# Optimization experiments

Measured on AMD Instinct MI355X. Metric: run time of the kernel, lower is better.

## Reference

```python
import jax, jax.numpy as jnp
import numpy as np

SCALE_BASE = 512.0
GN_EPS = 1e-5


def _xpos(x, downscale):
    # x: [..., L, D]; XPOS rotary embedding with exponential length scale (torchscale)
    L, D = x.shape[-2], x.shape[-1]
    half = D // 2
    base = (jnp.arange(0, D, 2, dtype=jnp.float32) + 0.4 * D) / (1.4 * D)  # [half]
    min_pos = -(L // 2)
    power = (jnp.arange(min_pos, min_pos + L, dtype=jnp.float32) / SCALE_BASE)[:, None]
    scale = base[None, :] ** power  # [L, half]
    inv_freq = 1.0 / (10000.0 ** (jnp.arange(half, dtype=jnp.float32) / half))
    ang = jnp.arange(L, dtype=jnp.float32)[:, None] * inv_freq[None, :]  # [L, half]
    sin, cos = jnp.sin(ang), jnp.cos(ang)
    if downscale:
        scale = 1.0 / scale
    sin_s = jnp.repeat(sin * scale, 2, axis=-1)  # duplicate_interleave -> [L, D]
    cos_s = jnp.repeat(cos * scale, 2, axis=-1)
    x1, x2 = x[..., ::2], x[..., 1::2]
    rot = jnp.stack((-x2, x1), axis=-1).reshape(x.shape)  # rotate_every_two
    return x * cos_s + rot * sin_s


def _decay_mask(L, H):
    gammas = 1.0 - jnp.exp(jnp.linspace(np.log(1.0 / 32.0), np.log(1.0 / 512.0), H)).astype(jnp.float32)
    idx = jnp.arange(L)
    dist = idx[:, None] - idx[None, :]  # [L, L]
    causal = dist >= 0
    d = jnp.maximum(dist, 0).astype(jnp.float32)
    # gamma^|n-s| below diagonal, 0 above (gamma^inf = 0 in the torch version)
    return jnp.where(causal[None], gammas[:, None, None] ** d[None], 0.0)  # [H, L, L]


def setup_inputs() -> dict:
    key = jax.random.key(0)
    ks = jax.random.split(key, 9)
    B, L, D, H = 2, 2048, 1024, 16
    hd = D // H
    return {
        "query": jax.random.normal(ks[0], (B, L, D), jnp.float32),
        "key": jax.random.normal(ks[1], (B, L, D), jnp.float32),
        "value": jax.random.normal(ks[2], (B, L, D), jnp.float32),
        "W_Q": jax.random.normal(ks[3], (H, D, hd), jnp.float32) / D,
        "W_K": jax.random.normal(ks[4], (H, D, hd), jnp.float32) / D,
        "W_V": jax.random.normal(ks[5], (H, D, hd), jnp.float32) / D,
        "g_w": jax.random.normal(ks[6], (D, D), jnp.float32) * (2.0 / (D + D)) ** 0.5,
        "g_b": jnp.zeros((D,), jnp.float32),
        "out_w": jax.random.normal(ks[7], (D, D), jnp.float32) * (2.0 / (D + D)) ** 0.5,
        "out_b": jnp.zeros((D,), jnp.float32),
    }


def reference(query, key, value, W_Q, W_K, W_V, g_w, g_b, out_w, out_b):
    B, L, D = query.shape
    H = W_Q.shape[0]
    q = jnp.einsum('bld,hde->bhle', query, W_Q)
    k = jnp.einsum('bld,hde->bhle', key, W_K)
    v = jnp.einsum('bld,hde->bhle', value, W_V)
    q = _xpos(q, downscale=False)
    k = _xpos(k, downscale=True)
    # retention_parallel: QK^T * decay mask (no softmax, no scale), then @ V
    sim = jnp.einsum('bhnd,bhsd->bhns', q, k) * _decay_mask(L, H)[None]
    ret = jnp.einsum('bhns,bhsd->bhnd', sim, v)  # [B, H, L, hd]
    # GroupNorm(num_groups=H, affine=False) on (b n, h d): normalize per (b, h, n) over hd
    mu = ret.mean(axis=-1, keepdims=True)
    var = ret.var(axis=-1, keepdims=True)
    ret = (ret - mu) / jnp.sqrt(var + GN_EPS)
    ret = ret.transpose(0, 2, 1, 3).reshape(B, L, D)  # b h n d -> b n (h d)
    gate = jax.nn.silu(query @ g_w.T + g_b)
    return (ret * gate) @ out_w.T + out_b
```

## Files before the change

### kernel.cpp

```cpp
#include <hip/hip_runtime.h>
#include <cstdint>

#define B_  2
#define L_  2048
#define D_  1024
#define H_  16
#define HD_ 64
#define M_  (B_*L_)

#define MD  4194304u
#define DD  1048576u

#define OFF_XQB  0u
#define OFF_XKB  (MD)
#define OFF_XVB  (2u*MD)
#define OFF_WQT  (3u*MD)
#define OFF_WKT  (3u*MD + DD)
#define OFF_WVT  (3u*MD + 2u*DD)
#define OFF_GWB  (3u*MD + 3u*DD)
#define OFF_OWB  (3u*MD + 4u*DD)
#define OFF_GATE (3u*MD + 5u*DD)
#define OFF_QB2  (OFF_GATE + MD)
#define OFF_KB2  (OFF_QB2 + MD)
#define OFF_VTG  (OFF_KB2 + MD)
#define OFF_ABUF (OFF_VTG + MD)
#define OFF_F32  (OFF_ABUF + MD)

typedef __attribute__((ext_vector_type(8))) short bf16x8;
typedef __attribute__((ext_vector_type(4))) float f32x4;

__device__ __forceinline__ unsigned short f2b(float x){
  union { float f; unsigned u; } a; a.f = x;
  unsigned r = a.u + 0x7FFFu + ((a.u >> 16) & 1u);
  return (unsigned short)(r >> 16);
}
__device__ __forceinline__ float b2f(unsigned short u){
  union { unsigned u; float f; } a; a.u = ((unsigned)u) << 16; return a.f;
}

__global__ __launch_bounds__(256) void cast_all_kernel(
    const float* __restrict__ q, const float* __restrict__ k,
    const float* __restrict__ v, const float* __restrict__ gw,
    const float* __restrict__ ow, unsigned short* __restrict__ ws)
{
  size_t i = ((size_t)blockIdx.x * 256 + threadIdx.x) * 4;
  const float* src; unsigned short* dst;
  if (i < MD)            { src = q  + i;              dst = ws + OFF_XQB + i; }
  else if (i < 2u*MD)    { src = k  + (i - MD);       dst = ws + OFF_XKB + (i - MD); }
  else if (i < 3u*MD)    { src = v  + (i - 2u*MD);    dst = ws + OFF_XVB + (i - 2u*MD); }
  else if (i < 3u*MD+DD) { src = gw + (i - 3u*MD);    dst = ws + OFF_GWB + (i - 3u*MD); }
  else                   { src = ow + (i - 3u*MD-DD); dst = ws + OFF_OWB + (i - 3u*MD - DD); }
  float4 vv = *(const float4*)src;
  ushort4 o; o.x = f2b(vv.x); o.y = f2b(vv.y); o.z = f2b(vv.z); o.w = f2b(vv.w);
  *(ushort4*)dst = o;
}

__global__ void transpose_w_kernel(const float* __restrict__ WQ,
                                   const float* __restrict__ WK,
                                   const float* __restrict__ WV,
                                   unsigned short* __restrict__ ws)
{
  __shared__ float t[32][33];
  const int z = blockIdx.z, w = z >> 4, h = z & 15;
  const float* in = (w == 0) ? WQ : (w == 1) ? WK : WV;
  unsigned short* out = ws + ((w == 0) ? OFF_WQT : (w == 1) ? OFF_WKT : OFF_WVT);
  const int d0 = blockIdx.x * 32, e0 = blockIdx.y * 32;
  const int x = threadIdx.x;
  for (int yy = threadIdx.y; yy < 32; yy += 8)
    t[yy][x] = in[((size_t)h * D_ + d0 + yy) * HD_ + e0 + x];
  __syncthreads();
  for (int yy = threadIdx.y; yy < 32; yy += 8)
    out[((size_t)h * HD_ + e0 + yy) * D_ + d0 + x] = f2b(t[x][yy]);
}

__global__ void xpos_tables_kernel(float* __restrict__ fb)
{
  const int l = blockIdx.x, i = threadIdx.x;
  const float base = (2.0f * (float)i + 0.4f * (float)HD_) / (1.4f * (float)HD_);
  const float p = (float)(l - L_ / 2) * (1.0f / 512.0f);
  const float sc = exp2f(p * log2f(base));
  const float invf = exp2f(-(float)i * (13.287712379549449f / 32.0f));
  float s, c; sincosf((float)l * invf, &s, &c);
  fb[          l * 32 + i] = c * sc;
  fb[ 65536 +  l * 32 + i] = s * sc;
  const float is = 1.0f / sc;
  fb[131072 +  l * 32 + i] = c * is;
  fb[196608 +  l * 32 + i] = s * is;
}

__device__ __forceinline__ void gemm_body(
    const unsigned short* __restrict__ A, const unsigned short* __restrict__ Bt,
    float* __restrict__ outF, unsigned short* __restrict__ outB,
    const float* __restrict__ ct, const float* __restrict__ st,
    const float* __restrict__ bias, int mode, int ldc, int M0, int N0,
    short* As, short* Bs)
{
  const int tid = threadIdx.x;
  const int wave = tid >> 6, lane = tid & 63;
  const int wm = wave & 1, wn = wave >> 1;
  const int mlane = lane & 15, kgrp = lane >> 4;
  const int arow0 = wave * 32 + (lane >> 2);
  const int akc   = lane & 3;
  const int brow  = wave * 16 + (lane >> 2);
  const char* Ab = (const char*)A;
  const char* Bb = (const char*)Bt;

  f32x4 acc[4][2] = {};

  for (int K0 = 0; K0 < 1024; K0 += 32) {
    __syncthreads();
#pragma unroll
    for (int t = 0; t < 2; ++t) {
      const char* g = Ab + ((size_t)(M0 + arow0 + t * 16) * 1024 + K0 + akc * 8) * 2;
      __builtin_amdgcn_global_load_lds(
          (const __attribute__((address_space(1))) void*)g,
          (__attribute__((address_space(3))) void*)((char*)As + (wave * 2 + t) * 1024 + lane * 16),
          16, 0, 0);
    }
    {
      const char* g = Bb + ((size_t)(N0 + brow) * 1024 + K0 + akc * 8) * 2;
      __builtin_amdgcn_global_load_lds(
          (const __attribute__((address_space(1))) void*)g,
          (__attribute__((address_space(3))) void*)((char*)Bs + wave * 1024 + lane * 16),
          16, 0, 0);
    }
    __syncthreads();
    bf16x8 af[4], bfr[2];
#pragma unroll
    for (int tm = 0; tm < 4; ++tm)
      af[tm] = *(const bf16x8*)&As[(wm * 64 + tm * 16 + mlane) * 32 + kgrp * 8];
#pragma unroll
    for (int tn = 0; tn < 2; ++tn)
      bfr[tn] = *(const bf16x8*)&Bs[(wn * 32 + tn * 16 + mlane) * 32 + kgrp * 8];
#pragma unroll
    for (int tm = 0; tm < 4; ++tm)
#pragma unroll
      for (int tn = 0; tn < 2; ++tn)
        acc[tm][tn] = __builtin_amdgcn_mfma_f32_16x16x32_bf16(af[tm], bfr[tn], acc[tm][tn], 0, 0, 0);
  }

#pragma unroll
  for (int tm = 0; tm < 4; ++tm)
#pragma unroll
    for (int tn = 0; tn < 2; ++tn) {
      f32x4 v = acc[tm][tn];
#pragma unroll
      for (int r = 0; r < 4; ++r) {
        const int grow = M0 + wm * 64 + tm * 16 + (lane >> 4) * 4 + r;
        const int gcol = N0 + wn * 32 + tn * 16 + mlane;
        float val = v[r];
        if (mode == 1 || mode == 2) {
          const float partner = __shfl_xor(val, 1);
          const int l = grow & (L_ - 1);
          const int i = (gcol >> 1) & 31;
          const float c = ct[l * 32 + i], s = st[l * 32 + i];
          val = (gcol & 1) ? (val * c + partner * s) : (val * c - partner * s);
          outB[(size_t)grow * ldc + gcol] = f2b(val);
        } else if (mode == 0) {
          outB[(size_t)grow * ldc + gcol] = f2b(val);
        } else if (mode == 3) {
          const float x = val + bias[gcol];
          outB[(size_t)grow * ldc + gcol] = f2b(x / (1.0f + expf(-x)));
        } else {
          outF[(size_t)grow * ldc + gcol] = val + bias[gcol];
        }
      }
    }
}

__global__ __launch_bounds__(256) void gemm4_kernel(
    unsigned short* __restrict__ ws, const float* __restrict__ g_b)
{
  __shared__ __align__(16) short As[128 * 32];
  __shared__ __align__(16) short Bs[64 * 32];
  const int z = blockIdx.y, bx = blockIdx.x;
  float* fb = (float*)(ws + OFF_F32);
  const unsigned short *A, *Bt; unsigned short* outB;
  const float *ct = nullptr, *st = nullptr, *bias = nullptr;
  int mode, ldc, M0, N0;
  if (z == 0) {
    A = ws + OFF_XQB; Bt = ws + OFF_WQT; outB = ws + OFF_QB2;
    ct = fb; st = fb + 65536; mode = 1; ldc = D_;
    M0 = (bx & 31) * 128; N0 = (bx >> 5) * 64;
  } else if (z == 1) {
    A = ws + OFF_XKB; Bt = ws + OFF_WKT; outB = ws + OFF_KB2;
    ct = fb + 131072; st = fb + 196608; mode = 2; ldc = D_;
    M0 = (bx & 31) * 128; N0 = (bx >> 5) * 64;
  } else if (z == 2) {
    A = ws + OFF_WVT; Bt = ws + OFF_XVB; outB = ws + OFF_VTG;
    mode = 0; ldc = M_;
    M0 = (bx & 7) * 128; N0 = (bx >> 3) * 64;
  } else {
    A = ws + OFF_XQB; Bt = ws + OFF_GWB; outB = ws + OFF_GATE;
    bias = g_b; mode = 3; ldc = D_;
    M0 = (bx & 31) * 128; N0 = (bx >> 5) * 64;
  }
  gemm_body(A, Bt, nullptr, outB, ct, st, bias, mode, ldc, M0, N0, As, Bs);
}

__global__ __launch_bounds__(256) void gemm_final_kernel(
    unsigned short* __restrict__ ws, const float* __restrict__ out_b,
    float* __restrict__ out)
{
  __shared__ __align__(16) short As[128 * 32];
  __shared__ __align__(16) short Bs[64 * 32];
  gemm_body(ws + OFF_ABUF, ws + OFF_OWB, out, nullptr, nullptr, nullptr,
            out_b, 4, D_, blockIdx.x * 128, blockIdx.y * 64, As, Bs);
}

#define QS_OFF 0
#define KS_OFF 16384
#define VT_OFF 24576
#define PS_OFF 32768

__global__ __launch_bounds__(256) void attn_mfma_kernel(
    const unsigned short* __restrict__ qg, const unsigned short* __restrict__ kg,
    const unsigned short* __restrict__ vtg, const unsigned short* __restrict__ gate,
    unsigned short* __restrict__ Abuf)
{
  __shared__ __align__(16) char smem[49152];
  const int tid = threadIdx.x, wave = tid >> 6, lane = tid & 63;
  const int mlane = lane & 15, kgrp = lane >> 4;
  const int id = blockIdx.x;
  const int bh = id & 31;
  const int u  = id >> 5;
  const int xq = (u < 8) ? u : (23 - u);
  const int l0 = xq * 128;
  const int b = bh >> 4, h = bh & 15;

  const float lo   = -3.4657359027997265f;
  const float step = -0.1848392481493187f;
  const float gamma = 1.0f - expf(lo + (float)h * step);
  const float lg2g  = log2f(gamma);
  const float g1    = exp2f(-lg2g);
  const float gmr[4] = {1.0f, g1, g1 * g1, g1 * g1 * g1};

  const int rl = lane >> 3, csel = lane & 7;

#pragma unroll
  for (int t = 0; t < 4; ++t) {
    const int row = 32 * wave + 8 * t + rl;
    const char* g = (const char*)(qg + (size_t)(b * L_ + l0 + row) * D_ + h * HD_ + ((csel ^ (row & 7)) << 3));
    __builtin_amdgcn_global_load_lds(
        (const __attribute__((address_space(1))) void*)g,
        (__attribute__((address_space(3))) void*)(smem + QS_OFF + (32 * wave + 8 * t) * 128 + lane * 16),
        16, 0, 0);
  }
  __syncthreads();

  bf16x8 qa[2][2];
#pragma unroll
  for (int tm = 0; tm < 2; ++tm)
#pragma unroll
    for (int kk = 0; kk < 2; ++kk) {
      const int row = 32 * wave + 16 * tm + mlane;
      qa[tm][kk] = *(const bf16x8*)(smem + QS_OFF + row * 128 + (((4 * kk + kgrp) ^ (row & 7)) << 4));
    }

  float rqm[2];
#pragma unroll
  for (int tm = 0; tm < 2; ++tm)
    rqm[tm] = exp2f((float)(l0 + 32 * wave + 16 * tm + mlane) * lg2g);

  f32x4 racc[2][4] = {};
  const int ntile = 2 * xq + 2;

  for (int it = 0; it < ntile; ++it) {
    const int s0 = it * 64;
    __syncthreads();
#pragma unroll
    for (int t = 0; t < 2; ++t) {
      const int row = 16 * wave + 8 * t + rl;
      const char* gk = (const char*)(kg + (size_t)(b * L_ + s0 + row) * D_ + h * HD_ + ((csel ^ (row & 7)) << 3));
      __builtin_amdgcn_global_load_lds(
          (const __attribute__((address_space(1))) void*)gk,
          (__attribute__((address_space(3))) void*)(smem + KS_OFF + (16 * wave + 8 * t) * 128 + lane * 16),
          16, 0, 0);
      const char* gv = (const char*)(vtg + (size_t)(h * HD_ + row) * M_ + b * L_ + s0 + ((csel ^ (row & 7)) << 3));
      __builtin_amdgcn_global_load_lds(
          (const __attribute__((address_space(1))) void*)gv,
          (__attribute__((address_space(3))) void*)(smem + VT_OFF + (16 * wave + 8 * t) * 128 + lane * 16),
          16, 0, 0);
    }
    __syncthreads();

    if (s0 <= l0 + 32 * wave + 31) {
      bf16x8 kb[4][2], vb[4][2];
#pragma unroll
      for (int tn = 0; tn < 4; ++tn)
#pragma unroll
        for (int kk = 0; kk < 2; ++kk) {
          const int row = 16 * tn + mlane;
          const int sw = ((4 * kk + kgrp) ^ (row & 7)) << 4;
          kb[tn][kk] = *(const bf16x8*)(smem + KS_OFF + row * 128 + sw);
          vb[tn][kk] = *(const bf16x8*)(smem + VT_OFF + row * 128 + sw);
        }
      float csb[4];
#pragma unroll
      for (int tn = 0; tn < 4; ++tn)
        csb[tn] = exp2f(-(float)(s0 + 16 * tn + 4 * kgrp) * lg2g);

#pragma unroll
      for (int tm = 0; tm < 2; ++tm) {
        const int rowmin = l0 + 32 * wave + 16 * tm;
        if (s0 > rowmin + 15) continue;
        f32x4 sf[4];
#pragma unroll
        for (int tn = 0; tn < 4; ++tn) {
          f32x4 z = {};
          z = __builtin_amdgcn_mfma_f32_16x16x32_bf16(kb[tn][0], qa[tm][0], z, 0, 0, 0);
          sf[tn] = __builtin_amdgcn_mfma_f32_16x16x32_bf16(kb[tn][1], qa[tm][1], z, 0, 0, 0);
        }
        const int nrow = rowmin + mlane;
        const bool needMask = (s0 + 63 >= rowmin);
        const int prow = 32 * wave + 16 * tm + mlane;
#pragma unroll
        for (int tn = 0; tn < 4; ++tn) {
          const float wbase = rqm[tm] * csb[tn];
          const int sbase = s0 + 16 * tn + 4 * kgrp;
          float vv[4];
#pragma unroll
          for (int r = 0; r < 4; ++r) {
            float w = wbase * gmr[r];
            if (needMask) w = (nrow - (sbase + r) >= 0) ? w : 0.0f;
            vv[r] = sf[tn][r] * w;
          }
          uint2 pk;
          pk.x = (unsigned)f2b(vv[0]) | ((unsigned)f2b(vv[1]) << 16);
          pk.y = (unsigned)f2b(vv[2]) | ((unsigned)f2b(vv[3]) << 16);
          *(uint2*)(smem + PS_OFF + prow * 128 +
                    (((2 * tn + (kgrp >> 1)) ^ (prow & 7)) << 4) + ((kgrp & 1) << 3)) = pk;
        }
        bf16x8 pa[2];
#pragma unroll
        for (int kk = 0; kk < 2; ++kk) {
          const int row = 32 * wave + 16 * tm + mlane;
          pa[kk] = *(const bf16x8*)(smem + PS_OFF + row * 128 + (((4 * kk + kgrp) ^ (row & 7)) << 4));
        }
#pragma unroll
        for (int tn = 0; tn < 4; ++tn) {
          racc[tm][tn] = __builtin_amdgcn_mfma_f32_16x16x32_bf16(pa[0], vb[tn][0], racc[tm][tn], 0, 0, 0);
          racc[tm][tn] = __builtin_amdgcn_mfma_f32_16x16x32_bf16(pa[1], vb[tn][1], racc[tm][tn], 0, 0, 0);
        }
      }
    }
  }

#pragma unroll
  for (int tm = 0; tm < 2; ++tm)
#pragma unroll
    for (int r = 0; r < 4; ++r) {
      float vv[4], sm = 0.0f, sq = 0.0f;
#pragma unroll
      for (int tn = 0; tn < 4; ++tn) {
        vv[tn] = racc[tm][tn][r];
        sm += vv[tn]; sq += vv[tn] * vv[tn];
      }
#pragma unroll
      for (int off = 1; off < 16; off <<= 1) {
        sm += __shfl_xor(sm, off);
        sq += __shfl_xor(sq, off);
      }
      const float mu = sm * (1.0f / 64.0f);
      float var = sq * (1.0f / 64.0f) - mu * mu;
      var = fmaxf(var, 0.0f);
      const float inv = rsqrtf(var + 1e-5f);
      const int row = l0 + 32 * wave + 16 * tm + kgrp * 4 + r;
      const size_t base = (size_t)(b * L_ + row) * D_ + h * HD_;
#pragma unroll
      for (int tn = 0; tn < 4; ++tn) {
        const int c = 16 * tn + mlane;
        const float g = b2f(gate[base + c]);
        Abuf[base + c] = f2b((vv[tn] - mu) * inv * g);
      }
    }
}

extern "C" void kernel_launch(void* const* d_in, const int* in_sizes, int n_in,
                              void* d_out, int out_size, void* d_ws, size_t ws_size,
                              hipStream_t stream)
{
  const float* query = (const float*)d_in[0];
  const float* key   = (const float*)d_in[1];
  const float* value = (const float*)d_in[2];
  const float* W_Q   = (const float*)d_in[3];
  const float* W_K   = (const float*)d_in[4];
  const float* W_V   = (const float*)d_in[5];
  const float* g_b   = (const float*)d_in[7];
  const float* out_b = (const float*)d_in[9];
  float* out = (float*)d_out;

  unsigned short* ws = (unsigned short*)d_ws;
  float* fb = (float*)(ws + OFF_F32);

  cast_all_kernel<<<14336, 256, 0, stream>>>(query, key, value,
                                             (const float*)d_in[6],
                                             (const float*)d_in[8], ws);
  transpose_w_kernel<<<dim3(32, 2, 48), dim3(32, 8), 0, stream>>>(W_Q, W_K, W_V, ws);
  xpos_tables_kernel<<<2048, 32, 0, stream>>>(fb);

  gemm4_kernel<<<dim3(512, 4), 256, 0, stream>>>(ws, g_b);

  attn_mfma_kernel<<<512, 256, 0, stream>>>(ws + OFF_QB2, ws + OFF_KB2,
                                            ws + OFF_VTG, ws + OFF_GATE,
                                            ws + OFF_ABUF);

  gemm_final_kernel<<<dim3(M_ / 128, D_ / 64), 256, 0, stream>>>(ws, out_b, out);
}
```

Before: 267.8 us.

## Fuse prep kernels, enlarge GEMM tiles to 128x128, persistent attention scheduler

Merges the cast, weight-transpose and xpos-table kernels into one launch to cut launch overhead. The GEMM tile grows from 128x64 to 128x128 with XOR-swizzled LDS to raise data reuse and avoid bank conflicts, at the cost of more accumulator registers and half as many blocks. Attention becomes a persistent kernel that takes 64-row query tiles from an atomic work counter, longest tiles first, to balance the causal triangle across CUs. The counter is reset inside the gemm4 kernel, which adds an ordering dependency between launches.

```diff
diff --git a/kernel.cpp b/kernel.cpp
--- a/kernel.cpp
+++ b/kernel.cpp
@@ -38,54 +38,55 @@
   union { unsigned u; float f; } a; a.u = ((unsigned)u) << 16; return a.f;
 }
 
-__global__ __launch_bounds__(256) void cast_all_kernel(
+__global__ __launch_bounds__(256) void prep_kernel(
     const float* __restrict__ q, const float* __restrict__ k,
     const float* __restrict__ v, const float* __restrict__ gw,
-    const float* __restrict__ ow, unsigned short* __restrict__ ws)
-{
-  size_t i = ((size_t)blockIdx.x * 256 + threadIdx.x) * 4;
-  const float* src; unsigned short* dst;
-  if (i < MD)            { src = q  + i;              dst = ws + OFF_XQB + i; }
-  else if (i < 2u*MD)    { src = k  + (i - MD);       dst = ws + OFF_XKB + (i - MD); }
-  else if (i < 3u*MD)    { src = v  + (i - 2u*MD);    dst = ws + OFF_XVB + (i - 2u*MD); }
-  else if (i < 3u*MD+DD) { src = gw + (i - 3u*MD);    dst = ws + OFF_GWB + (i - 3u*MD); }
-  else                   { src = ow + (i - 3u*MD-DD); dst = ws + OFF_OWB + (i - 3u*MD - DD); }
-  float4 vv = *(const float4*)src;
-  ushort4 o; o.x = f2b(vv.x); o.y = f2b(vv.y); o.z = f2b(vv.z); o.w = f2b(vv.w);
-  *(ushort4*)dst = o;
-}
-
-__global__ void transpose_w_kernel(const float* __restrict__ WQ,
-                                   const float* __restrict__ WK,
-                                   const float* __restrict__ WV,
-                                   unsigned short* __restrict__ ws)
+    const float* __restrict__ ow, const float* __restrict__ WQ,
+    const float* __restrict__ WK, const float* __restrict__ WV,
+    unsigned short* __restrict__ ws)
 {
   __shared__ float t[32][33];
-  const int z = blockIdx.z, w = z >> 4, h = z & 15;
-  const float* in = (w == 0) ? WQ : (w == 1) ? WK : WV;
-  unsigned short* out = ws + ((w == 0) ? OFF_WQT : (w == 1) ? OFF_WKT : OFF_WVT);
-  const int d0 = blockIdx.x * 32, e0 = blockIdx.y * 32;
-  const int x = threadIdx.x;
-  for (int yy = threadIdx.y; yy < 32; yy += 8)
-    t[yy][x] = in[((size_t)h * D_ + d0 + yy) * HD_ + e0 + x];
-  __syncthreads();
-  for (int yy = threadIdx.y; yy < 32; yy += 8)
-    out[((size_t)h * HD_ + e0 + yy) * D_ + d0 + x] = f2b(t[x][yy]);
-}
-
-__global__ void xpos_tables_kernel(float* __restrict__ fb)
-{
-  const int l = blockIdx.x, i = threadIdx.x;
-  const float base = (2.0f * (float)i + 0.4f * (float)HD_) / (1.4f * (float)HD_);
-  const float p = (float)(l - L_ / 2) * (1.0f / 512.0f);
-  const float sc = exp2f(p * log2f(base));
-  const float invf = exp2f(-(float)i * (13.287712379549449f / 32.0f));
-  float s, c; sincosf((float)l * invf, &s, &c);
-  fb[          l * 32 + i] = c * sc;
-  fb[ 65536 +  l * 32 + i] = s * sc;
-  const float is = 1.0f / sc;
-  fb[131072 +  l * 32 + i] = c * is;
-  fb[196608 +  l * 32 + i] = s * is;
+  const int bx = blockIdx.x, tid = threadIdx.x;
+  if (bx < 14336) {
+    size_t i = ((size_t)bx * 256 + tid) * 4;
+    const float* src; unsigned short* dst;
+    if (i < MD)            { src = q  + i;              dst = ws + OFF_XQB + i; }
+    else if (i < 2u*MD)    { src = k  + (i - MD);       dst = ws + OFF_XKB + (i - MD); }
+    else if (i < 3u*MD)    { src = v  + (i - 2u*MD);    dst = ws + OFF_XVB + (i - 2u*MD); }
+    else if (i < 3u*MD+DD) { src = gw + (i - 3u*MD);    dst = ws + OFF_GWB + (i - 3u*MD); }
+    else                   { src = ow + (i - 3u*MD-DD); dst = ws + OFF_OWB + (i - 3u*MD - DD); }
+    float4 vv = *(const float4*)src;
+    ushort4 o; o.x = f2b(vv.x); o.y = f2b(vv.y); o.z = f2b(vv.z); o.w = f2b(vv.w);
+    *(ushort4*)dst = o;
+  } else if (bx < 17408) {
+    const int tb = bx - 14336;
+    const int w = tb >> 10;
+    const int tb2 = tb & 1023;
+    const int h = tb2 >> 6, tt = tb2 & 63;
+    const int e0 = (tt & 1) * 32, d0 = (tt >> 1) * 32;
+    const float* in = (w == 0) ? WQ : (w == 1) ? WK : WV;
+    unsigned short* out = ws + ((w == 0) ? OFF_WQT : (w == 1) ? OFF_WKT : OFF_WVT);
+    const int x = tid & 31, y0 = tid >> 5;
+    for (int yy = y0; yy < 32; yy += 8)
+      t[yy][x] = in[((size_t)h * D_ + d0 + yy) * HD_ + e0 + x];
+    __syncthreads();
+    for (int yy = y0; yy < 32; yy += 8)
+      out[((size_t)h * HD_ + e0 + yy) * D_ + d0 + x] = f2b(t[x][yy]);
+  } else {
+    float* fb = (float*)(ws + OFF_F32);
+    const int idx = (bx - 17408) * 256 + tid;
+    const int l = idx >> 5, i = idx & 31;
+    const float base = (2.0f * (float)i + 0.4f * (float)HD_) / (1.4f * (float)HD_);
+    const float p = (float)(l - L_ / 2) * (1.0f / 512.0f);
+    const float sc = exp2f(p * log2f(base));
+    const float invf = exp2f(-(float)i * (13.287712379549449f / 32.0f));
+    float s, c; sincosf((float)l * invf, &s, &c);
+    fb[          l * 32 + i] = c * sc;
+    fb[ 65536 +  l * 32 + i] = s * sc;
+    const float is = 1.0f / sc;
+    fb[131072 +  l * 32 + i] = c * is;
+    fb[196608 +  l * 32 + i] = s * is;
+  }
 }
 
 __device__ __forceinline__ void gemm_body(
@@ -93,61 +94,64 @@
     float* __restrict__ outF, unsigned short* __restrict__ outB,
     const float* __restrict__ ct, const float* __restrict__ st,
     const float* __restrict__ bias, int mode, int ldc, int M0, int N0,
-    short* As, short* Bs)
+    char* As, char* Bs)
 {
   const int tid = threadIdx.x;
   const int wave = tid >> 6, lane = tid & 63;
   const int wm = wave & 1, wn = wave >> 1;
   const int mlane = lane & 15, kgrp = lane >> 4;
-  const int arow0 = wave * 32 + (lane >> 2);
-  const int akc   = lane & 3;
-  const int brow  = wave * 16 + (lane >> 2);
+  const int srow = lane >> 2;
+  const int scs  = lane & 3;
   const char* Ab = (const char*)A;
   const char* Bb = (const char*)Bt;
 
-  f32x4 acc[4][2] = {};
+  f32x4 acc[4][4] = {};
 
   for (int K0 = 0; K0 < 1024; K0 += 32) {
     __syncthreads();
 #pragma unroll
     for (int t = 0; t < 2; ++t) {
-      const char* g = Ab + ((size_t)(M0 + arow0 + t * 16) * 1024 + K0 + akc * 8) * 2;
+      const int row = wave * 32 + t * 16 + srow;
+      const int gc = scs ^ ((row >> 1) & 3);
+      const char* ga = Ab + ((size_t)(M0 + row) * 1024 + K0 + gc * 8) * 2;
       __builtin_amdgcn_global_load_lds(
-          (const __attribute__((address_space(1))) void*)g,
-          (__attribute__((address_space(3))) void*)((char*)As + (wave * 2 + t) * 1024 + lane * 16),
+          (const __attribute__((address_space(1))) void*)ga,
+          (__attribute__((address_space(3))) void*)(As + (wave * 32 + t * 16) * 64 + lane * 16),
           16, 0, 0);
-    }
-    {
-      const char* g = Bb + ((size_t)(N0 + brow) * 1024 + K0 + akc * 8) * 2;
+      const char* gb = Bb + ((size_t)(N0 + row) * 1024 + K0 + gc * 8) * 2;
       __builtin_amdgcn_global_load_lds(
-          (const __attribute__((address_space(1))) void*)g,
-          (__attribute__((address_space(3))) void*)((char*)Bs + wave * 1024 + lane * 16),
+          (const __attribute__((address_space(1))) void*)gb,
+          (__attribute__((address_space(3))) void*)(Bs + (wave * 32 + t * 16) * 64 + lane * 16),
           16, 0, 0);
     }
     __syncthreads();
-    bf16x8 af[4], bfr[2];
+    bf16x8 af[4], bfr[4];
+#pragma unroll
+    for (int tm = 0; tm < 4; ++tm) {
+      const int r = wm * 64 + tm * 16 + mlane;
+      af[tm] = *(const bf16x8*)(As + r * 64 + ((kgrp ^ ((r >> 1) & 3)) << 4));
+    }
+#pragma unroll
+    for (int tn = 0; tn < 4; ++tn) {
+      const int r = wn * 64 + tn * 16 + mlane;
+      bfr[tn] = *(const bf16x8*)(Bs + r * 64 + ((kgrp ^ ((r >> 1) & 3)) << 4));
+    }
 #pragma unroll
     for (int tm = 0; tm < 4; ++tm)
-      af[tm] = *(const bf16x8*)&As[(wm * 64 + tm * 16 + mlane) * 32 + kgrp * 8];
-#pragma unroll
-    for (int tn = 0; tn < 2; ++tn)
-      bfr[tn] = *(const bf16x8*)&Bs[(wn * 32 + tn * 16 + mlane) * 32 + kgrp * 8];
-#pragma unroll
-    for (int tm = 0; tm < 4; ++tm)
-#pragma unroll
-      for (int tn = 0; tn < 2; ++tn)
+#pragma unroll
+      for (int tn = 0; tn < 4; ++tn)
         acc[tm][tn] = __builtin_amdgcn_mfma_f32_16x16x32_bf16(af[tm], bfr[tn], acc[tm][tn], 0, 0, 0);
   }
 
 #pragma unroll
   for (int tm = 0; tm < 4; ++tm)
 #pragma unroll
-    for (int tn = 0; tn < 2; ++tn) {
+    for (int tn = 0; tn < 4; ++tn) {
       f32x4 v = acc[tm][tn];
 #pragma unroll
       for (int r = 0; r < 4; ++r) {
         const int grow = M0 + wm * 64 + tm * 16 + (lane >> 4) * 4 + r;
-        const int gcol = N0 + wn * 32 + tn * 16 + mlane;
+        const int gcol = N0 + wn * 64 + tn * 16 + mlane;
         float val = v[r];
         if (mode == 1 || mode == 2) {
           const float partner = __shfl_xor(val, 1);
@@ -171,29 +175,31 @@
 __global__ __launch_bounds__(256) void gemm4_kernel(
     unsigned short* __restrict__ ws, const float* __restrict__ g_b)
 {
-  __shared__ __align__(16) short As[128 * 32];
-  __shared__ __align__(16) short Bs[64 * 32];
+  __shared__ __align__(16) char As[128 * 64];
+  __shared__ __align__(16) char Bs[128 * 64];
   const int z = blockIdx.y, bx = blockIdx.x;
   float* fb = (float*)(ws + OFF_F32);
+  if (z == 0 && bx == 0 && threadIdx.x == 0)
+    ((unsigned*)(fb + 262144))[0] = 0;
   const unsigned short *A, *Bt; unsigned short* outB;
   const float *ct = nullptr, *st = nullptr, *bias = nullptr;
   int mode, ldc, M0, N0;
   if (z == 0) {
     A = ws + OFF_XQB; Bt = ws + OFF_WQT; outB = ws + OFF_QB2;
     ct = fb; st = fb + 65536; mode = 1; ldc = D_;
-    M0 = (bx & 31) * 128; N0 = (bx >> 5) * 64;
+    M0 = (bx & 31) * 128; N0 = (bx >> 5) * 128;
   } else if (z == 1) {
     A = ws + OFF_XKB; Bt = ws + OFF_WKT; outB = ws + OFF_KB2;
     ct = fb + 131072; st = fb + 196608; mode = 2; ldc = D_;
-    M0 = (bx & 31) * 128; N0 = (bx >> 5) * 64;
+    M0 = (bx & 31) * 128; N0 = (bx >> 5) * 128;
   } else if (z == 2) {
     A = ws + OFF_WVT; Bt = ws + OFF_XVB; outB = ws + OFF_VTG;
     mode = 0; ldc = M_;
-    M0 = (bx & 7) * 128; N0 = (bx >> 3) * 64;
+    M0 = (bx & 7) * 128; N0 = (bx >> 3) * 128;
   } else {
     A = ws + OFF_XQB; Bt = ws + OFF_GWB; outB = ws + OFF_GATE;
     bias = g_b; mode = 3; ldc = D_;
-    M0 = (bx & 31) * 128; N0 = (bx >> 5) * 64;
+    M0 = (bx & 31) * 128; N0 = (bx >> 5) * 128;
   }
   gemm_body(A, Bt, nullptr, outB, ct, st, bias, mode, ldc, M0, N0, As, Bs);
 }
@@ -202,89 +208,87 @@
     unsigned short* __restrict__ ws, const float* __restrict__ out_b,
     float* __restrict__ out)
 {
-  __shared__ __align__(16) short As[128 * 32];
-  __shared__ __align__(16) short Bs[64 * 32];
+  __shared__ __align__(16) char As[128 * 64];
+  __shared__ __align__(16) char Bs[128 * 64];
   gemm_body(ws + OFF_ABUF, ws + OFF_OWB, out, nullptr, nullptr, nullptr,
-            out_b, 4, D_, blockIdx.x * 128, blockIdx.y * 64, As, Bs);
-}
-
-#define QS_OFF 0
-#define KS_OFF 16384
-#define VT_OFF 24576
-#define PS_OFF 32768
+            out_b, 4, D_, blockIdx.x * 128, blockIdx.y * 128, As, Bs);
+}
+
+#define AQ_OFF 0
+#define AK_OFF 8192
+#define AV_OFF 16384
+#define AP_OFF 24576
 
 __global__ __launch_bounds__(256) void attn_mfma_kernel(
     const unsigned short* __restrict__ qg, const unsigned short* __restrict__ kg,
     const unsigned short* __restrict__ vtg, const unsigned short* __restrict__ gate,
-    unsigned short* __restrict__ Abuf)
-{
-  __shared__ __align__(16) char smem[49152];
+    unsigned short* __restrict__ Abuf, unsigned* __restrict__ ctr)
+{
+  __shared__ __align__(16) char smem[32768];
+  __shared__ unsigned s_item;
   const int tid = threadIdx.x, wave = tid >> 6, lane = tid & 63;
   const int mlane = lane & 15, kgrp = lane >> 4;
-  const int id = blockIdx.x;
-  const int bh = id & 31;
-  const int u  = id >> 5;
-  const int xq = (u < 8) ? u : (23 - u);
-  const int l0 = xq * 128;
-  const int b = bh >> 4, h = bh & 15;
+  const int rl = lane >> 3, csel = lane & 7;
 
   const float lo   = -3.4657359027997265f;
   const float step = -0.1848392481493187f;
-  const float gamma = 1.0f - expf(lo + (float)h * step);
-  const float lg2g  = log2f(gamma);
-  const float g1    = exp2f(-lg2g);
-  const float gmr[4] = {1.0f, g1, g1 * g1, g1 * g1 * g1};
-
-  const int rl = lane >> 3, csel = lane & 7;
-
-#pragma unroll
-  for (int t = 0; t < 4; ++t) {
-    const int row = 32 * wave + 8 * t + rl;
-    const char* g = (const char*)(qg + (size_t)(b * L_ + l0 + row) * D_ + h * HD_ + ((csel ^ (row & 7)) << 3));
-    __builtin_amdgcn_global_load_lds(
-        (const __attribute__((address_space(1))) void*)g,
-        (__attribute__((address_space(3))) void*)(smem + QS_OFF + (32 * wave + 8 * t) * 128 + lane * 16),
-        16, 0, 0);
-  }
-  __syncthreads();
-
-  bf16x8 qa[2][2];
-#pragma unroll
-  for (int tm = 0; tm < 2; ++tm)
-#pragma unroll
-    for (int kk = 0; kk < 2; ++kk) {
-      const int row = 32 * wave + 16 * tm + mlane;
-      qa[tm][kk] = *(const bf16x8*)(smem + QS_OFF + row * 128 + (((4 * kk + kgrp) ^ (row & 7)) << 4));
-    }
-
-  float rqm[2];
-#pragma unroll
-  for (int tm = 0; tm < 2; ++tm)
-    rqm[tm] = exp2f((float)(l0 + 32 * wave + 16 * tm + mlane) * lg2g);
-
-  f32x4 racc[2][4] = {};
-  const int ntile = 2 * xq + 2;
-
-  for (int it = 0; it < ntile; ++it) {
-    const int s0 = it * 64;
-    __syncthreads();
+
+  for (;;) {
+    __syncthreads();
+    if (tid == 0) s_item = atomicAdd(ctr, 1u);
+    __syncthreads();
+    const unsigned j = s_item;
+    if (j >= 1024u) break;
+    const int xq = 31 - (int)(j >> 5);
+    const int bh = (int)(j & 31u), b = bh >> 4, h = bh & 15;
+    const int l0 = xq * 64;
+
+    const float gamma = 1.0f - expf(lo + (float)h * step);
+    const float lg2g  = log2f(gamma);
+    const float g1    = exp2f(-lg2g);
+    const float gmr[4] = {1.0f, g1, g1 * g1, g1 * g1 * g1};
+
 #pragma unroll
     for (int t = 0; t < 2; ++t) {
       const int row = 16 * wave + 8 * t + rl;
-      const char* gk = (const char*)(kg + (size_t)(b * L_ + s0 + row) * D_ + h * HD_ + ((csel ^ (row & 7)) << 3));
+      const char* g = (const char*)(qg + (size_t)(b * L_ + l0 + row) * D_ + h * HD_ + ((csel ^ (row & 7)) << 3));
       __builtin_amdgcn_global_load_lds(
-          (const __attribute__((address_space(1))) void*)gk,
-          (__attribute__((address_space(3))) void*)(smem + KS_OFF + (16 * wave + 8 * t) * 128 + lane * 16),
+          (const __attribute__((address_space(1))) void*)g,
+          (__attribute__((address_space(3))) void*)(smem + AQ_OFF + (16 * wave + 8 * t) * 128 + lane * 16),
           16, 0, 0);
-      const char* gv = (const char*)(vtg + (size_t)(h * HD_ + row) * M_ + b * L_ + s0 + ((csel ^ (row & 7)) << 3));
-      __builtin_amdgcn_global_load_lds(
-          (const __attribute__((address_space(1))) void*)gv,
-          (__attribute__((address_space(3))) void*)(smem + VT_OFF + (16 * wave + 8 * t) * 128 + lane * 16),
-          16, 0, 0);
-    }
-    __syncthreads();
-
-    if (s0 <= l0 + 32 * wave + 31) {
+    }
+    __syncthreads();
+
+    bf16x8 qa[2];
+    {
+      const int row = 16 * wave + mlane;
+#pragma unroll
+      for (int kk = 0; kk < 2; ++kk)
+        qa[kk] = *(const bf16x8*)(smem + AQ_OFF + row * 128 + (((4 * kk + kgrp) ^ (row & 7)) << 4));
+    }
+    const float rqm = exp2f((float)(l0 + 16 * wave + mlane) * lg2g);
+
+    f32x4 racc[4] = {};
+
+    for (int it = 0; it <= xq; ++it) {
+      const int s0 = it * 64;
+      __syncthreads();
+#pragma unroll
+      for (int t = 0; t < 2; ++t) {
+        const int row = 16 * wave + 8 * t + rl;
+        const char* gk = (const char*)(kg + (size_t)(b * L_ + s0 + row) * D_ + h * HD_ + ((csel ^ (row & 7)) << 3));
+        __builtin_amdgcn_global_load_lds(
+            (const __attribute__((address_space(1))) void*)gk,
+            (__attribute__((address_space(3))) void*)(smem + AK_OFF + (16 * wave + 8 * t) * 128 + lane * 16),
+            16, 0, 0);
+        const char* gv = (const char*)(vtg + (size_t)(h * HD_ + row) * M_ + b * L_ + s0 + ((csel ^ (row & 7)) << 3));
+        __builtin_amdgcn_global_load_lds(
+            (const __attribute__((address_space(1))) void*)gv,
+            (__attribute__((address_space(3))) void*)(smem + AV_OFF + (16 * wave + 8 * t) * 128 + lane * 16),
+            16, 0, 0);
+      }
+      __syncthreads();
+
       bf16x8 kb[4][2], vb[4][2];
 #pragma unroll
       for (int tn = 0; tn < 4; ++tn)
@@ -292,68 +296,60 @@
         for (int kk = 0; kk < 2; ++kk) {
           const int row = 16 * tn + mlane;
           const int sw = ((4 * kk + kgrp) ^ (row & 7)) << 4;
-          kb[tn][kk] = *(const bf16x8*)(smem + KS_OFF + row * 128 + sw);
-          vb[tn][kk] = *(const bf16x8*)(smem + VT_OFF + row * 128 + sw);
+          kb[tn][kk] = *(const bf16x8*)(smem + AK_OFF + row * 128 + sw);
+          vb[tn][kk] = *(const bf16x8*)(smem + AV_OFF + row * 128 + sw);
         }
       float csb[4];
 #pragma unroll
       for (int tn = 0; tn < 4; ++tn)
         csb[tn] = exp2f(-(float)(s0 + 16 * tn + 4 * kgrp) * lg2g);
 
-#pragma unroll
-      for (int tm = 0; tm < 2; ++tm) {
-        const int rowmin = l0 + 32 * wave + 16 * tm;
-        if (s0 > rowmin + 15) continue;
-        f32x4 sf[4];
-#pragma unroll
-        for (int tn = 0; tn < 4; ++tn) {
-          f32x4 z = {};
-          z = __builtin_amdgcn_mfma_f32_16x16x32_bf16(kb[tn][0], qa[tm][0], z, 0, 0, 0);
-          sf[tn] = __builtin_amdgcn_mfma_f32_16x16x32_bf16(kb[tn][1], qa[tm][1], z, 0, 0, 0);
+      f32x4 sf[4];
+#pragma unroll
+      for (int tn = 0; tn < 4; ++tn) {
+        f32x4 z = {};
+        z = __builtin_amdgcn_mfma_f32_16x16x32_bf16(kb[tn][0], qa[0], z, 0, 0, 0);
+        sf[tn] = __builtin_amdgcn_mfma_f32_16x16x32_bf16(kb[tn][1], qa[1], z, 0, 0, 0);
+      }
+      const int nrow = l0 + 16 * wave + mlane;
+      const bool needMask = (it == xq);
+      const int prow = 16 * wave + mlane;
+#pragma unroll
+      for (int tn = 0; tn < 4; ++tn) {
+        const float wbase = rqm * csb[tn];
+        const int sbase = s0 + 16 * tn + 4 * kgrp;
+        float vv[4];
+#pragma unroll
+        for (int r = 0; r < 4; ++r) {
+          float w = wbase * gmr[r];
+          if (needMask) w = (nrow - (sbase + r) >= 0) ? w : 0.0f;
+          vv[r] = sf[tn][r] * w;
         }
-        const int nrow = rowmin + mlane;
-        const bool needMask = (s0 + 63 >= rowmin);
-        const int prow = 32 * wave + 16 * tm + mlane;
-#pragma unroll
-        for (int tn = 0; tn < 4; ++tn) {
-          const float wbase = rqm[tm] * csb[tn];
-          const int sbase = s0 + 16 * tn + 4 * kgrp;
-          float vv[4];
-#pragma unroll
-          for (int r = 0; r < 4; ++r) {
-            float w = wbase * gmr[r];
-            if (needMask) w = (nrow - (sbase + r) >= 0) ? w : 0.0f;
-            vv[r] = sf[tn][r] * w;
-          }
-          uint2 pk;
-          pk.x = (unsigned)f2b(vv[0]) | ((unsigned)f2b(vv[1]) << 16);
-          pk.y = (unsigned)f2b(vv[2]) | ((unsigned)f2b(vv[3]) << 16);
-          *(uint2*)(smem + PS_OFF + prow * 128 +
-                    (((2 * tn + (kgrp >> 1)) ^ (prow & 7)) << 4) + ((kgrp & 1) << 3)) = pk;
-        }
-        bf16x8 pa[2];
-#pragma unroll
-        for (int kk = 0; kk < 2; ++kk) {
-          const int row = 32 * wave + 16 * tm + mlane;
-          pa[kk] = *(const bf16x8*)(smem + PS_OFF + row * 128 + (((4 * kk + kgrp) ^ (row & 7)) << 4));
-        }
-#pragma unroll
-        for (int tn = 0; tn < 4; ++tn) {
-          racc[tm][tn] = __builtin_amdgcn_mfma_f32_16x16x32_bf16(pa[0], vb[tn][0], racc[tm][tn], 0, 0, 0);
-          racc[tm][tn] = __builtin_amdgcn_mfma_f32_16x16x32_bf16(pa[1], vb[tn][1], racc[tm][tn], 0, 0, 0);
-        }
-      }
-    }
-  }
-
-#pragma unroll
-  for (int tm = 0; tm < 2; ++tm)
+        uint2 pk;
+        pk.x = (unsigned)f2b(vv[0]) | ((unsigned)f2b(vv[1]) << 16);
+        pk.y = (unsigned)f2b(vv[2]) | ((unsigned)f2b(vv[3]) << 16);
+        *(uint2*)(smem + AP_OFF + prow * 128 +
+                  (((2 * tn + (kgrp >> 1)) ^ (prow & 7)) << 4) + ((kgrp & 1) << 3)) = pk;
+      }
+      bf16x8 pa[2];
+#pragma unroll
+      for (int kk = 0; kk < 2; ++kk) {
+        const int row = 16 * wave + mlane;
+        pa[kk] = *(const bf16x8*)(smem + AP_OFF + row * 128 + (((4 * kk + kgrp) ^ (row & 7)) << 4));
+      }
+#pragma unroll
+      for (int tn = 0; tn < 4; ++tn) {
+        racc[tn] = __builtin_amdgcn_mfma_f32_16x16x32_bf16(pa[0], vb[tn][0], racc[tn], 0, 0, 0);
+        racc[tn] = __builtin_amdgcn_mfma_f32_16x16x32_bf16(pa[1], vb[tn][1], racc[tn], 0, 0, 0);
+      }
+    }
+
 #pragma unroll
     for (int r = 0; r < 4; ++r) {
       float vv[4], sm = 0.0f, sq = 0.0f;
 #pragma unroll
       for (int tn = 0; tn < 4; ++tn) {
-        vv[tn] = racc[tm][tn][r];
+        vv[tn] = racc[tn][r];
         sm += vv[tn]; sq += vv[tn] * vv[tn];
       }
 #pragma unroll
@@ -365,7 +361,7 @@
       float var = sq * (1.0f / 64.0f) - mu * mu;
       var = fmaxf(var, 0.0f);
       const float inv = rsqrtf(var + 1e-5f);
-      const int row = l0 + 32 * wave + 16 * tm + kgrp * 4 + r;
+      const int row = l0 + 16 * wave + kgrp * 4 + r;
       const size_t base = (size_t)(b * L_ + row) * D_ + h * HD_;
 #pragma unroll
       for (int tn = 0; tn < 4; ++tn) {
@@ -374,6 +370,7 @@
         Abuf[base + c] = f2b((vv[tn] - mu) * inv * g);
       }
     }
+  }
 }
 
 extern "C" void kernel_launch(void* const* d_in, const int* in_sizes, int n_in,
@@ -392,18 +389,18 @@
 
   unsigned short* ws = (unsigned short*)d_ws;
   float* fb = (float*)(ws + OFF_F32);
-
-  cast_all_kernel<<<14336, 256, 0, stream>>>(query, key, value,
-                                             (const float*)d_in[6],
-                                             (const float*)d_in[8], ws);
-  transpose_w_kernel<<<dim3(32, 2, 48), dim3(32, 8), 0, stream>>>(W_Q, W_K, W_V, ws);
-  xpos_tables_kernel<<<2048, 32, 0, stream>>>(fb);
-
-  gemm4_kernel<<<dim3(512, 4), 256, 0, stream>>>(ws, g_b);
+  unsigned* ctr = (unsigned*)(fb + 262144);
+
+  prep_kernel<<<17664, 256, 0, stream>>>(query, key, value,
+                                         (const float*)d_in[6],
+                                         (const float*)d_in[8],
+                                         W_Q, W_K, W_V, ws);
+
+  gemm4_kernel<<<dim3(256, 4), 256, 0, stream>>>(ws, g_b);
 
   attn_mfma_kernel<<<512, 256, 0, stream>>>(ws + OFF_QB2, ws + OFF_KB2,
                                             ws + OFF_VTG, ws + OFF_GATE,
-                                            ws + OFF_ABUF);
-
-  gemm_final_kernel<<<dim3(M_ / 128, D_ / 64), 256, 0, stream>>>(ws, out_b, out);
-}
+                                            ws + OFF_ABUF, ctr);
+
+  gemm_final_kernel<<<dim3(32, 8), 256, 0, stream>>>(ws, out_b, out);
+}
```

After: 268.7 us. About the same (+0.4%).
